# Kernel tuning notes

Measured on AMD Instinct MI355X. Metric: run time of the kernel, lower is better.

## Reference

```python
import jax, jax.numpy as jnp
import numpy as np

ALPHA = 10.0
DELTA = 0.0005
N = 16777216  # array_length


def setup_inputs() -> dict:
    key = jax.random.key(0)
    k1, k2 = jax.random.split(key)
    # learned parameter: in the original module this is initialized to linspace(0,1,N);
    # we use uniform [0,1] so the piecewise-linear search path is non-degenerate.
    indices = jax.random.uniform(k1, (N,), dtype=jnp.float32)
    array = jax.random.normal(k2, (N,), dtype=jnp.float32)
    return {"indices": indices, "array": array}


def reference(indices, array):
    # clamp learned knot positions to [0, 1]
    clamped = jnp.clip(indices, 0.0, 1.0)
    # piecewise-linear function f with x-knots = clamped, y-values = array.
    # jnp.interp requires ascending knots, so sort (x, y) pairs by x.
    order = jnp.argsort(clamped)
    xs = clamped[order]
    ys = array[order]
    # vectorized version of the per-index loop:
    #   left_item = f(clamped[i-1] + delta), this_item = f(clamped[i] - delta)
    q_left = clamped[:-1] + DELTA   # [N-1]
    q_this = clamped[1:] - DELTA    # [N-1]
    f_left = jnp.interp(q_left, xs, ys)
    f_this = jnp.interp(q_this, xs, ys)
    gap = jnp.maximum(f_left - f_this, 0.0)
    return ALPHA * jnp.sum(gap)
```

## Files before the change

### kernel.cpp

```cpp
#include <hip/hip_runtime.h>
#include <stdint.h>

#define ALPHA_C 10.0f
#define DELTA_C 0.0005f

typedef unsigned long long u64;
typedef unsigned u32;
typedef unsigned short u16;

#define KB2   (1u << 21)
#define NREG  8192
#define FPR   256
#define CAP   4096
#define DQ    137438953ULL
#define Q38MAX ((1ULL << 38) - 1)

#define OLDKB (1u << 22)
#define SCAN_BLOCKS 1024
#define SCAN_TPB 256
#define SCAN_PER_THREAD 16

__device__ __forceinline__ float clamp01(float x) {
    return fminf(fmaxf(x, 0.0f), 1.0f);
}
__device__ __forceinline__ u64 q38_of(float x) {
    double d = (double)clamp01(x) * 274877906944.0;
    u64 q = (u64)d;
    return q > Q38MAX ? Q38MAX : q;
}
__device__ __forceinline__ u16 f2bf(float f) {
    u32 b = __float_as_uint(f);
    return (u16)((b + 0x8000u) >> 16);
}
__device__ __forceinline__ float bf2f(u32 h) {
    return __uint_as_float(h << 16);
}


__global__ void __launch_bounds__(256) k_hist(const float* __restrict__ ind,
                                              u32* __restrict__ cnt8k, int n) {
    __shared__ u32 lh[NREG];
    for (int k = threadIdx.x; k < (int)NREG; k += 256) lh[k] = 0;
    __syncthreads();
    int stride = gridDim.x * blockDim.x;
    for (int i = blockIdx.x * blockDim.x + threadIdx.x; i < n; i += stride)
        atomicAdd(&lh[(u32)(q38_of(ind[i]) >> 25)], 1u);
    __syncthreads();
    for (int k = threadIdx.x; k < (int)NREG; k += 256) {
        u32 v = lh[k];
        if (v) atomicAdd(&cnt8k[k], v);
    }
}

__global__ void __launch_bounds__(1024) k_scan8k(u32* __restrict__ cnt8k) {
    __shared__ u32 lds[1024];
    int tid = threadIdx.x;
    int base = tid * 8;
    u32 v[8]; u32 tot = 0;
#pragma unroll
    for (int k = 0; k < 8; ++k) { v[k] = cnt8k[base + k]; tot += v[k]; }
    lds[tid] = tot;
    __syncthreads();
    u32 x = tot;
    for (int s = 1; s < 1024; s <<= 1) {
        u32 y = (tid >= s) ? lds[tid - s] : 0u;
        __syncthreads();
        x += y; lds[tid] = x;
        __syncthreads();
    }
    u32 run = x - tot;
#pragma unroll
    for (int k = 0; k < 8; ++k) { u32 c = v[k]; cnt8k[base + k] = run; run += c; }
}

__global__ void k_coarse(const float* __restrict__ ind, const float* __restrict__ arr,
                         u32* __restrict__ cnt8k,
                         u32* __restrict__ recx, u64* __restrict__ reciy, int n) {
    int i = blockIdx.x * blockDim.x + threadIdx.x;
    if (i < n) {
        float x = ind[i];
        u32 r = (u32)(q38_of(x) >> 25);
        u32 e = atomicAdd(&cnt8k[r], 1u);
        recx[e] = __float_as_uint(x);
        reciy[e] = ((u64)(u32)i << 16) | (u64)f2bf(arr[i]);
    }
}

__global__ void __launch_bounds__(256) k_fine(const u32* __restrict__ cnt8k,
                                              u32* __restrict__ foff,
                                              const u32* __restrict__ recx,
                                              u64* __restrict__ reciy_fdata) {
    __shared__ u32 sx[CAP];
    __shared__ u64 siy[CAP];
    __shared__ u32 incl[FPR];
    __shared__ u32 lexcl[FPR];
    __shared__ u32 lcnt[FPR];
    int r = blockIdx.x;
    u32 s = (r == 0) ? 0u : cnt8k[r - 1];
    u32 e = cnt8k[r];
    u32 cnt = e - s; if (cnt > CAP) cnt = CAP;
    for (u32 j = threadIdx.x; j < cnt; j += 256) { sx[j] = recx[s + j]; siy[j] = reciy_fdata[s + j]; }
    incl[threadIdx.x] = 0;
    lcnt[threadIdx.x] = 0;
    __syncthreads();
    for (u32 j = threadIdx.x; j < cnt; j += 256) {
        u32 lb = (u32)((q38_of(__uint_as_float(sx[j])) >> 17) & 255u);
        atomicAdd(&incl[lb], 1u);
    }
    __syncthreads();
    u32 myc = incl[threadIdx.x];
    u32 x = myc;
    for (int st = 1; st < 256; st <<= 1) {
        u32 y = (threadIdx.x >= (u32)st) ? incl[threadIdx.x - st] : 0u;
        __syncthreads();
        x += y; incl[threadIdx.x] = x;
        __syncthreads();
    }
    lexcl[threadIdx.x] = x - myc;
    foff[r * FPR + threadIdx.x] = s + x;
    __syncthreads();
    for (u32 j = threadIdx.x; j < cnt; j += 256) {
        u64 q = q38_of(__uint_as_float(sx[j]));
        u32 lb = (u32)((q >> 17) & 255u);
        u32 p = s + lexcl[lb] + atomicAdd(&lcnt[lb], 1u);
        u64 iy = siy[j];
        reciy_fdata[p] = ((q & 0x1FFFFULL) << 40) | ((iy & 0xFFFFULL) << 24) | (iy >> 16);
    }
}

__device__ float feval_q(u64 q, const u32* __restrict__ foff, const u64* __restrict__ fdata) {
    u32 qb = (u32)(q >> 17);
    u32 ql = (u32)(q & 0x1FFFFu);
    u32 s = qb ? foff[qb - 1] : 0u;
    u32 e = foff[qb];
    long long loQ = -1;
    u64 hiQ = ~0ULL;
    float loY = 0.0f, hiY = 0.0f;
    for (u32 p = s; p < e; ++p) {
        u64 d = fdata[p];
        u32 xlo = (u32)(d >> 40);
        u64 eq = ((u64)qb << 17) | xlo;
        float y = bf2f((u32)(d >> 24) & 0xFFFFu);
        if (xlo <= ql) { if ((long long)eq >= loQ) { loQ = (long long)eq; loY = y; } }
        else           { if (eq < hiQ)             { hiQ = eq;            hiY = y; } }
    }
    if (loQ < 0) {
        u32 bl = qb;
        while (bl > 0) {
            --bl;
            u32 s2 = bl ? foff[bl - 1] : 0u;
            u32 e2 = foff[bl];
            if (e2 > s2) {
                for (u32 p = s2; p < e2; ++p) {
                    u64 d = fdata[p];
                    u64 eq = ((u64)bl << 17) | (d >> 40);
                    if ((long long)eq >= loQ) { loQ = (long long)eq; loY = bf2f((u32)(d >> 24) & 0xFFFFu); }
                }
                break;
            }
        }
    }
    if (hiQ == ~0ULL) {
        u32 br = qb;
        while (br < KB2 - 1) {
            ++br;
            u32 s2 = foff[br - 1];
            u32 e2 = foff[br];
            if (e2 > s2) {
                for (u32 p = s2; p < e2; ++p) {
                    u64 d = fdata[p];
                    u64 eq = ((u64)br << 17) | (d >> 40);
                    if (eq < hiQ) { hiQ = eq; hiY = bf2f((u32)(d >> 24) & 0xFFFFu); }
                }
                break;
            }
        }
    }
    if (loQ < 0) return hiY;
    if (hiQ == ~0ULL) return loY;
    float dq = (float)(q - (u64)loQ);
    float dd = (float)(hiQ - (u64)loQ);
    return loY + (dq / dd) * (hiY - loY);
}

__global__ void __launch_bounds__(256) k_eval_t1(const u32* __restrict__ cnt8k,
        const u32* __restrict__ foff, const u64* __restrict__ fdata,
        u32* __restrict__ obcnt, u64* __restrict__ orec, float* __restrict__ fmEdge) {
    __shared__ u32 fend[FPR];
    int r = blockIdx.x;
    u32 s = r ? cnt8k[r - 1] : 0u;
    u32 e = cnt8k[r];
    fend[threadIdx.x] = foff[r * FPR + threadIdx.x];
    __syncthreads();
    for (u32 t = s + threadIdx.x; t < e; t += 256) {
        u64 d = fdata[t];
        u32 lo = 0;
#pragma unroll
        for (u32 st = 128; st; st >>= 1) if (t >= fend[lo + st - 1]) lo += st;
        u64 xq = (((u64)((u32)r * FPR + lo)) << 17) | (d >> 40);
        u32 i = (u32)(d & 0xFFFFFFu);
        u64 qp = xq + DQ; if (qp > Q38MAX) qp = Q38MAX;
        u64 qm = (xq >= DQ) ? xq - DQ : 0ULL;
        float fp = feval_q(qp, foff, fdata);
        float fm = feval_q(qm, foff, fdata);
        u32 bin = i >> 11;
        u32 sl = atomicAdd(&obcnt[bin], 1u);
        orec[((u64)bin << 11) + sl] = ((u64)i << 32) | ((u64)f2bf(fp) << 16) | (u64)f2bf(fm);
        if ((i & 2047u) == 0u) fmEdge[bin] = fm;
    }
}

__global__ void __launch_bounds__(256) k_eval_t2(const u32* __restrict__ cnt8k,
        const u32* __restrict__ foff, const u64* __restrict__ fdata,
        u32* __restrict__ oval) {
    __shared__ u32 fend[FPR];
    int r = blockIdx.x;
    u32 s = r ? cnt8k[r - 1] : 0u;
    u32 e = cnt8k[r];
    fend[threadIdx.x] = foff[r * FPR + threadIdx.x];
    __syncthreads();
    for (u32 t = s + threadIdx.x; t < e; t += 256) {
        u64 d = fdata[t];
        u32 lo = 0;
#pragma unroll
        for (u32 st = 128; st; st >>= 1) if (t >= fend[lo + st - 1]) lo += st;
        u64 xq = (((u64)((u32)r * FPR + lo)) << 17) | (d >> 40);
        u32 i = (u32)(d & 0xFFFFFFu);
        u64 qp = xq + DQ; if (qp > Q38MAX) qp = Q38MAX;
        u64 qm = (xq >= DQ) ? xq - DQ : 0ULL;
        float fp = feval_q(qp, foff, fdata);
        float fm = feval_q(qm, foff, fdata);
        oval[i] = ((u32)f2bf(fp) << 16) | (u32)f2bf(fm);
    }
}

__global__ void __launch_bounds__(256) k_pair1(const u64* __restrict__ orec,
        const float* __restrict__ fmEdge, float* __restrict__ out, int n) {
    __shared__ u32 v[2048];
    int r = blockIdx.x;
    long long base = (long long)r << 11;
    int cap = (int)((long long)n - base); if (cap > 2048) cap = 2048;
    for (int k = threadIdx.x; k < cap; k += 256) {
        u64 d = orec[base + k];
        v[(u32)(d >> 32) & 2047u] = (u32)d;
    }
    __syncthreads();
    float sum = 0.0f;
    for (int k = threadIdx.x; k < cap; k += 256) {
        long long gi = base + k;
        if (gi <= (long long)n - 2) {
            float fp = bf2f(v[k] >> 16);
            float fm = (k < 2047) ? bf2f(v[k + 1] & 0xFFFFu) : fmEdge[r + 1];
            sum += fmaxf(fp - fm, 0.0f);
        }
    }
    float w = sum;
    for (int s = 32; s > 0; s >>= 1) w += __shfl_down(w, s, 64);
    __shared__ float wsum[4];
    if ((threadIdx.x & 63) == 0) wsum[threadIdx.x >> 6] = w;
    __syncthreads();
    if (threadIdx.x == 0)
        atomicAdd(out, ALPHA_C * (wsum[0] + wsum[1] + wsum[2] + wsum[3]));
}

__global__ void __launch_bounds__(256) k_pair2(const u32* __restrict__ oval,
                                               float* __restrict__ out, int n) {
    int stride = gridDim.x * blockDim.x;
    float sum = 0.0f;
    for (int j = blockIdx.x * blockDim.x + threadIdx.x; j < n - 1; j += stride) {
        u32 a = oval[j], b = oval[j + 1];
        sum += fmaxf(bf2f(a >> 16) - bf2f(b & 0xFFFFu), 0.0f);
    }
    float w = sum;
    for (int s = 32; s > 0; s >>= 1) w += __shfl_down(w, s, 64);
    __shared__ float wsum[4];
    if ((threadIdx.x & 63) == 0) wsum[threadIdx.x >> 6] = w;
    __syncthreads();
    if (threadIdx.x == 0)
        atomicAdd(out, ALPHA_C * (wsum[0] + wsum[1] + wsum[2] + wsum[3]));
}


__device__ __forceinline__ int bucket_of(float x) {
    int b = (int)(x * (float)OLDKB);
    b = b < 0 ? 0 : b;
    b = b > (int)OLDKB - 1 ? (int)OLDKB - 1 : b;
    return b;
}

__global__ void scan1(u32* __restrict__ off, u32* __restrict__ bsums) {
    __shared__ u32 lds[SCAN_TPB];
    int base = blockIdx.x * (SCAN_TPB * SCAN_PER_THREAD) + threadIdx.x * SCAN_PER_THREAD;
    u32 v[SCAN_PER_THREAD];
    u32 tot = 0;
#pragma unroll
    for (int k = 0; k < SCAN_PER_THREAD; ++k) { v[k] = off[base + k]; tot += v[k]; }
    lds[threadIdx.x] = tot;
    __syncthreads();
    u32 x = tot;
    for (int s = 1; s < SCAN_TPB; s <<= 1) {
        u32 y = (threadIdx.x >= (u32)s) ? lds[threadIdx.x - s] : 0u;
        __syncthreads();
        x += y; lds[threadIdx.x] = x;
        __syncthreads();
    }
    if (threadIdx.x == SCAN_TPB - 1) bsums[blockIdx.x] = x;
    u32 run = x - tot;
#pragma unroll
    for (int k = 0; k < SCAN_PER_THREAD; ++k) { u32 c = v[k]; off[base + k] = run; run += c; }
}

__global__ void scan2(u32* __restrict__ bsums) {
    __shared__ u32 lds[SCAN_BLOCKS];
    int tid = threadIdx.x;
    u32 v = bsums[tid];
    lds[tid] = v;
    __syncthreads();
    u32 x = v;
    for (int s = 1; s < SCAN_BLOCKS; s <<= 1) {
        u32 y = (tid >= s) ? lds[tid - s] : 0u;
        __syncthreads();
        x += y; lds[tid] = x;
        __syncthreads();
    }
    bsums[tid] = x - v;
}

__global__ void scan3(u32* __restrict__ off, const u32* __restrict__ bsums) {
    int base = blockIdx.x * (SCAN_TPB * SCAN_PER_THREAD);
    u32 add = bsums[blockIdx.x];
#pragma unroll
    for (int k = 0; k < SCAN_PER_THREAD; ++k)
        off[base + k * SCAN_TPB + threadIdx.x] += add;
}

__global__ void hist_kernel(const float* __restrict__ ind, u32* __restrict__ off, int n) {
    int i = blockIdx.x * blockDim.x + threadIdx.x;
    if (i < n) atomicAdd(&off[bucket_of(clamp01(ind[i]))], 1u);
}

__global__ void scatter_kernel(const float* __restrict__ ind, const float* __restrict__ arr,
                               u32* __restrict__ off, float2* __restrict__ buck, int n) {
    int i = blockIdx.x * blockDim.x + threadIdx.x;
    if (i < n) {
        float x = clamp01(ind[i]);
        u32 p = atomicAdd(&off[bucket_of(x)], 1u);
        buck[p] = make_float2(x, arr[i]);
    }
}

__device__ float feval(float q, const u32* __restrict__ off, const float2* __restrict__ buck) {
    int b = bucket_of(q);
    u32 s = (b == 0) ? 0u : off[b - 1];
    u32 e = off[b];
    float loX = -1e30f, loY = 0.0f, hiX = 1e30f, hiY = 0.0f;
    for (u32 u = s; u < e; ++u) {
        float2 p = buck[u];
        if (p.x <= q) { if (p.x >= loX) { loX = p.x; loY = p.y; } }
        else          { if (p.x <  hiX) { hiX = p.x; hiY = p.y; } }
    }
    if (loX == -1e30f) {
        int bl = b;
        while (bl > 0) {
            --bl;
            u32 s2 = (bl == 0) ? 0u : off[bl - 1];
            u32 e2 = off[bl];
            if (e2 > s2) {
                for (u32 u = s2; u < e2; ++u) {
                    float2 p = buck[u];
                    if (p.x >= loX) { loX = p.x; loY = p.y; }
                }
                break;
            }
        }
    }
    if (hiX == 1e30f) {
        int br = b;
        while (br < (int)OLDKB - 1) {
            ++br;
            u32 s2 = off[br - 1];
            u32 e2 = off[br];
            if (e2 > s2) {
                for (u32 u = s2; u < e2; ++u) {
                    float2 p = buck[u];
                    if (p.x < hiX) { hiX = p.x; hiY = p.y; }
                }
                break;
            }
        }
    }
    if (loX == -1e30f) return hiY;
    if (hiX ==  1e30f) return loY;
    return loY + (q - loX) * (hiY - loY) / (hiX - loX);
}

__global__ void query_kernel(const float* __restrict__ ind, const u32* __restrict__ off,
                             const float2* __restrict__ buck, float* __restrict__ out, int nterm) {
    int j = blockIdx.x * blockDim.x + threadIdx.x;
    float term = 0.0f;
    if (j < nterm) {
        float c0 = clamp01(ind[j]);
        float c1 = clamp01(ind[j + 1]);
        float fa = feval(c0 + DELTA_C, off, buck);
        float fb = feval(c1 - DELTA_C, off, buck);
        term = fmaxf(fa - fb, 0.0f);
    }
    float w = term;
    for (int s = 32; s > 0; s >>= 1) w += __shfl_down(w, s, 64);
    __shared__ float wsum[4];
    if ((threadIdx.x & 63) == 0) wsum[threadIdx.x >> 6] = w;
    __syncthreads();
    if (threadIdx.x == 0) atomicAdd(out, ALPHA_C * (wsum[0] + wsum[1] + wsum[2] + wsum[3]));
}


extern "C" void kernel_launch(void* const* d_in, const int* in_sizes, int n_in,
                              void* d_out, int out_size, void* d_ws, size_t ws_size,
                              hipStream_t stream) {
    const float* ind = (const float*)d_in[0];
    const float* arr = (const float*)d_in[1];
    float* out = (float*)d_out;
    int n = in_sizes[0];

    const int tpb = 256;
    int nblk = (n + tpb - 1) / tpb;
    uint8_t* w = (uint8_t*)d_ws;

    const size_t FOFF_SZ = (size_t)KB2 * 4;
    const size_t AUX = (size_t)1 << 20;
    size_t SZ8 = (size_t)n * 8, SZ4 = (size_t)n * 4;
    size_t base = FOFF_SZ + AUX;
    size_t need_t2 = base + SZ8 + SZ4;
    size_t need_t1 = base + SZ8 + SZ8;

    if (n <= (1 << 24) && ws_size >= need_t2) {
        u32* foff   = (u32*)w;
        u32* cnt8k  = (u32*)(w + FOFF_SZ);
        u32* obcnt  = (u32*)(w + FOFF_SZ + 65536);
        float* fmEdge = (float*)(w + FOFF_SZ + 131072);
        u64* reciy  = (u64*)(w + base);
        u32* recx   = (u32*)(w + base + SZ8);
        u64* orec   = (u64*)recx;
        u32* oval   = (u32*)recx;

        bool t1 = (ws_size >= need_t1);

        hipMemsetAsync(cnt8k, 0, NREG * 4, stream);
        if (t1) hipMemsetAsync(obcnt, 0, NREG * 4, stream);
        hipMemsetAsync(out, 0, sizeof(float) * (size_t)out_size, stream);

        k_hist<<<512, 256, 0, stream>>>(ind, cnt8k, n);
        k_scan8k<<<1, 1024, 0, stream>>>(cnt8k);
        k_coarse<<<nblk, tpb, 0, stream>>>(ind, arr, cnt8k, recx, reciy, n);
        k_fine<<<NREG, 256, 0, stream>>>(cnt8k, foff, recx, reciy);
        if (t1) {
            k_eval_t1<<<NREG, 256, 0, stream>>>(cnt8k, foff, reciy, obcnt, orec, fmEdge);
            int nbins = (n + 2047) / 2048;
            k_pair1<<<nbins, 256, 0, stream>>>(orec, fmEdge, out, n);
        } else {
            k_eval_t2<<<NREG, 256, 0, stream>>>(cnt8k, foff, reciy, oval);
            k_pair2<<<2048, 256, 0, stream>>>(oval, out, n);
        }
    } else {
        const size_t FO = (size_t)OLDKB * 4;
        u32* off = (u32*)w;
        u32* bsums = (u32*)(w + FO);
        float2* buck = (float2*)(w + FO + 4096);

        hipMemsetAsync(off, 0, FO, stream);
        hipMemsetAsync(out, 0, sizeof(float) * (size_t)out_size, stream);

        hist_kernel<<<nblk, tpb, 0, stream>>>(ind, off, n);
        scan1<<<SCAN_BLOCKS, SCAN_TPB, 0, stream>>>(off, bsums);
        scan2<<<1, SCAN_BLOCKS, 0, stream>>>(bsums);
        scan3<<<SCAN_BLOCKS, SCAN_TPB, 0, stream>>>(off, bsums);
        scatter_kernel<<<nblk, tpb, 0, stream>>>(ind, arr, off, buck, n);
        int nterm = n - 1;
        query_kernel<<<(nterm + tpb - 1) / tpb, tpb, 0, stream>>>(ind, off, buck, out, nterm);
    }
}
```

Measured before the change: 1.742 ms.

## Double fine buckets, store 16-bit bucket offsets, drop scattered-output eval path

Doubles the number of fine buckets per region to 512, so each interpolation lookup scans fewer records, and stores the per-bucket offsets as 16-bit values relative to the region base. It also drops the t1 path (atomic binning plus the pair1 kernel) in favour of always writing oval directly and running pair2. Query points are now computed in float (x ± delta) instead of with a fixed-point delta, and ties are broken by index in the key to better match the reference. The costs are an extra cnt8k lookup per bucket range, 512-thread blocks in k_fine and k_eval, and a random scatter on the oval write.

```diff
diff --git a/kernel.cpp b/kernel.cpp
--- a/kernel.cpp
+++ b/kernel.cpp
@@ -8,11 +8,10 @@
 typedef unsigned u32;
 typedef unsigned short u16;
 
-#define KB2   (1u << 21)
+#define KB2   (1u << 22)
 #define NREG  8192
-#define FPR   256
+#define FPR   512
 #define CAP   4096
-#define DQ    137438953ULL
 #define Q38MAX ((1ULL << 38) - 1)
 
 #define OLDKB (1u << 22)
@@ -86,8 +85,8 @@
     }
 }
 
-__global__ void __launch_bounds__(256) k_fine(const u32* __restrict__ cnt8k,
-                                              u32* __restrict__ foff,
+__global__ void __launch_bounds__(512) k_fine(const u32* __restrict__ cnt8k,
+                                              u16* __restrict__ foff16,
                                               const u32* __restrict__ recx,
                                               u64* __restrict__ reciy_fdata) {
     __shared__ u32 sx[CAP];
@@ -99,168 +98,129 @@
     u32 s = (r == 0) ? 0u : cnt8k[r - 1];
     u32 e = cnt8k[r];
     u32 cnt = e - s; if (cnt > CAP) cnt = CAP;
-    for (u32 j = threadIdx.x; j < cnt; j += 256) { sx[j] = recx[s + j]; siy[j] = reciy_fdata[s + j]; }
+    for (u32 j = threadIdx.x; j < cnt; j += 512) { sx[j] = recx[s + j]; siy[j] = reciy_fdata[s + j]; }
     incl[threadIdx.x] = 0;
     lcnt[threadIdx.x] = 0;
     __syncthreads();
-    for (u32 j = threadIdx.x; j < cnt; j += 256) {
-        u32 lb = (u32)((q38_of(__uint_as_float(sx[j])) >> 17) & 255u);
+    for (u32 j = threadIdx.x; j < cnt; j += 512) {
+        u32 lb = (u32)((q38_of(__uint_as_float(sx[j])) >> 16) & (FPR - 1));
         atomicAdd(&incl[lb], 1u);
     }
     __syncthreads();
     u32 myc = incl[threadIdx.x];
     u32 x = myc;
-    for (int st = 1; st < 256; st <<= 1) {
+    for (int st = 1; st < FPR; st <<= 1) {
         u32 y = (threadIdx.x >= (u32)st) ? incl[threadIdx.x - st] : 0u;
         __syncthreads();
         x += y; incl[threadIdx.x] = x;
         __syncthreads();
     }
     lexcl[threadIdx.x] = x - myc;
-    foff[r * FPR + threadIdx.x] = s + x;
-    __syncthreads();
-    for (u32 j = threadIdx.x; j < cnt; j += 256) {
+    foff16[r * FPR + threadIdx.x] = (u16)x;
+    __syncthreads();
+    for (u32 j = threadIdx.x; j < cnt; j += 512) {
         u64 q = q38_of(__uint_as_float(sx[j]));
-        u32 lb = (u32)((q >> 17) & 255u);
+        u32 lb = (u32)((q >> 16) & (FPR - 1));
         u32 p = s + lexcl[lb] + atomicAdd(&lcnt[lb], 1u);
         u64 iy = siy[j];
-        reciy_fdata[p] = ((q & 0x1FFFFULL) << 40) | ((iy & 0xFFFFULL) << 24) | (iy >> 16);
-    }
-}
-
-__device__ float feval_q(u64 q, const u32* __restrict__ foff, const u64* __restrict__ fdata) {
-    u32 qb = (u32)(q >> 17);
-    u32 ql = (u32)(q & 0x1FFFFu);
-    u32 s = qb ? foff[qb - 1] : 0u;
-    u32 e = foff[qb];
-    long long loQ = -1;
-    u64 hiQ = ~0ULL;
+        reciy_fdata[p] = ((q & 0xFFFFULL) << 40) | ((iy & 0xFFFFULL) << 24) | (iy >> 16);
+    }
+}
+
+__device__ __forceinline__ void bucket_range(u32 b, const u32* __restrict__ cnt8k,
+                                             const u16* __restrict__ foff16,
+                                             u32* s, u32* e) {
+    u32 r = b >> 9;
+    u32 rbase = r ? cnt8k[r - 1] : 0u;
+    u32 lb = b & (FPR - 1);
+    *s = rbase + (lb ? (u32)foff16[b - 1] : 0u);
+    *e = rbase + (u32)foff16[b];
+}
+
+__device__ float feval_q(u64 qq, const u32* __restrict__ cnt8k,
+                         const u16* __restrict__ foff16, const u64* __restrict__ fdata) {
+    u32 qb = (u32)(qq >> 16);
+    u32 ql = (u32)(qq & 0xFFFFu);
+    u32 s, e;
+    bucket_range(qb, cnt8k, foff16, &s, &e);
+    long long loK = -1;
+    u64 hiK = ~0ULL;
     float loY = 0.0f, hiY = 0.0f;
     for (u32 p = s; p < e; ++p) {
         u64 d = fdata[p];
         u32 xlo = (u32)(d >> 40);
-        u64 eq = ((u64)qb << 17) | xlo;
+        u64 key = ((((u64)qb << 16) | xlo) << 24) | (d & 0xFFFFFFULL);
         float y = bf2f((u32)(d >> 24) & 0xFFFFu);
-        if (xlo <= ql) { if ((long long)eq >= loQ) { loQ = (long long)eq; loY = y; } }
-        else           { if (eq < hiQ)             { hiQ = eq;            hiY = y; } }
-    }
-    if (loQ < 0) {
+        if (xlo <= ql) { if ((long long)key >= loK) { loK = (long long)key; loY = y; } }
+        else           { if (key < hiK)             { hiK = key;            hiY = y; } }
+    }
+    if (loK < 0) {
         u32 bl = qb;
         while (bl > 0) {
             --bl;
-            u32 s2 = bl ? foff[bl - 1] : 0u;
-            u32 e2 = foff[bl];
+            u32 s2, e2;
+            bucket_range(bl, cnt8k, foff16, &s2, &e2);
             if (e2 > s2) {
                 for (u32 p = s2; p < e2; ++p) {
                     u64 d = fdata[p];
-                    u64 eq = ((u64)bl << 17) | (d >> 40);
-                    if ((long long)eq >= loQ) { loQ = (long long)eq; loY = bf2f((u32)(d >> 24) & 0xFFFFu); }
+                    u64 key = ((((u64)bl << 16) | (d >> 40)) << 24) | (d & 0xFFFFFFULL);
+                    if ((long long)key >= loK) { loK = (long long)key; loY = bf2f((u32)(d >> 24) & 0xFFFFu); }
                 }
                 break;
             }
         }
     }
-    if (hiQ == ~0ULL) {
+    if (hiK == ~0ULL) {
         u32 br = qb;
         while (br < KB2 - 1) {
             ++br;
-            u32 s2 = foff[br - 1];
-            u32 e2 = foff[br];
+            u32 s2, e2;
+            bucket_range(br, cnt8k, foff16, &s2, &e2);
             if (e2 > s2) {
                 for (u32 p = s2; p < e2; ++p) {
                     u64 d = fdata[p];
-                    u64 eq = ((u64)br << 17) | (d >> 40);
-                    if (eq < hiQ) { hiQ = eq; hiY = bf2f((u32)(d >> 24) & 0xFFFFu); }
+                    u64 key = ((((u64)br << 16) | (d >> 40)) << 24) | (d & 0xFFFFFFULL);
+                    if (key < hiK) { hiK = key; hiY = bf2f((u32)(d >> 24) & 0xFFFFu); }
                 }
                 break;
             }
         }
     }
-    if (loQ < 0) return hiY;
-    if (hiQ == ~0ULL) return loY;
-    float dq = (float)(q - (u64)loQ);
-    float dd = (float)(hiQ - (u64)loQ);
+    if (loK < 0) return hiY;
+    if (hiK == ~0ULL) return loY;
+    u64 loQ = (u64)loK >> 24;
+    u64 hiQ = hiK >> 24;
+    if (hiQ == loQ) return loY;
+    float dq = (float)(qq - loQ);
+    float dd = (float)(hiQ - loQ);
     return loY + (dq / dd) * (hiY - loY);
 }
 
-__global__ void __launch_bounds__(256) k_eval_t1(const u32* __restrict__ cnt8k,
-        const u32* __restrict__ foff, const u64* __restrict__ fdata,
-        u32* __restrict__ obcnt, u64* __restrict__ orec, float* __restrict__ fmEdge) {
-    __shared__ u32 fend[FPR];
-    int r = blockIdx.x;
-    u32 s = r ? cnt8k[r - 1] : 0u;
-    u32 e = cnt8k[r];
-    fend[threadIdx.x] = foff[r * FPR + threadIdx.x];
-    __syncthreads();
-    for (u32 t = s + threadIdx.x; t < e; t += 256) {
-        u64 d = fdata[t];
-        u32 lo = 0;
-#pragma unroll
-        for (u32 st = 128; st; st >>= 1) if (t >= fend[lo + st - 1]) lo += st;
-        u64 xq = (((u64)((u32)r * FPR + lo)) << 17) | (d >> 40);
-        u32 i = (u32)(d & 0xFFFFFFu);
-        u64 qp = xq + DQ; if (qp > Q38MAX) qp = Q38MAX;
-        u64 qm = (xq >= DQ) ? xq - DQ : 0ULL;
-        float fp = feval_q(qp, foff, fdata);
-        float fm = feval_q(qm, foff, fdata);
-        u32 bin = i >> 11;
-        u32 sl = atomicAdd(&obcnt[bin], 1u);
-        orec[((u64)bin << 11) + sl] = ((u64)i << 32) | ((u64)f2bf(fp) << 16) | (u64)f2bf(fm);
-        if ((i & 2047u) == 0u) fmEdge[bin] = fm;
-    }
-}
-
-__global__ void __launch_bounds__(256) k_eval_t2(const u32* __restrict__ cnt8k,
-        const u32* __restrict__ foff, const u64* __restrict__ fdata,
+__global__ void __launch_bounds__(512) k_eval(const u32* __restrict__ cnt8k,
+        const u16* __restrict__ foff16, const u64* __restrict__ fdata,
         u32* __restrict__ oval) {
     __shared__ u32 fend[FPR];
     int r = blockIdx.x;
     u32 s = r ? cnt8k[r - 1] : 0u;
     u32 e = cnt8k[r];
-    fend[threadIdx.x] = foff[r * FPR + threadIdx.x];
-    __syncthreads();
-    for (u32 t = s + threadIdx.x; t < e; t += 256) {
+    fend[threadIdx.x] = s + (u32)foff16[r * FPR + threadIdx.x];
+    __syncthreads();
+    for (u32 t = s + threadIdx.x; t < e; t += 512) {
         u64 d = fdata[t];
         u32 lo = 0;
 #pragma unroll
-        for (u32 st = 128; st; st >>= 1) if (t >= fend[lo + st - 1]) lo += st;
-        u64 xq = (((u64)((u32)r * FPR + lo)) << 17) | (d >> 40);
+        for (u32 st = 256; st; st >>= 1) if (t >= fend[lo + st - 1]) lo += st;
+        u64 xq = (((u64)((u32)r * FPR + lo)) << 16) | (d >> 40);
         u32 i = (u32)(d & 0xFFFFFFu);
-        u64 qp = xq + DQ; if (qp > Q38MAX) qp = Q38MAX;
-        u64 qm = (xq >= DQ) ? xq - DQ : 0ULL;
-        float fp = feval_q(qp, foff, fdata);
-        float fm = feval_q(qm, foff, fdata);
+        float x = (float)((double)xq * 3.63797880709171295e-12);
+        float qpf = x + DELTA_C;
+        float qmf = x - DELTA_C;
+        u64 qp = q38_of(qpf);
+        u64 qm = q38_of(qmf);
+        float fp = feval_q(qp, cnt8k, foff16, fdata);
+        float fm = feval_q(qm, cnt8k, foff16, fdata);
         oval[i] = ((u32)f2bf(fp) << 16) | (u32)f2bf(fm);
     }
-}
-
-__global__ void __launch_bounds__(256) k_pair1(const u64* __restrict__ orec,
-        const float* __restrict__ fmEdge, float* __restrict__ out, int n) {
-    __shared__ u32 v[2048];
-    int r = blockIdx.x;
-    long long base = (long long)r << 11;
-    int cap = (int)((long long)n - base); if (cap > 2048) cap = 2048;
-    for (int k = threadIdx.x; k < cap; k += 256) {
-        u64 d = orec[base + k];
-        v[(u32)(d >> 32) & 2047u] = (u32)d;
-    }
-    __syncthreads();
-    float sum = 0.0f;
-    for (int k = threadIdx.x; k < cap; k += 256) {
-        long long gi = base + k;
-        if (gi <= (long long)n - 2) {
-            float fp = bf2f(v[k] >> 16);
-            float fm = (k < 2047) ? bf2f(v[k + 1] & 0xFFFFu) : fmEdge[r + 1];
-            sum += fmaxf(fp - fm, 0.0f);
-        }
-    }
-    float w = sum;
-    for (int s = 32; s > 0; s >>= 1) w += __shfl_down(w, s, 64);
-    __shared__ float wsum[4];
-    if ((threadIdx.x & 63) == 0) wsum[threadIdx.x >> 6] = w;
-    __syncthreads();
-    if (threadIdx.x == 0)
-        atomicAdd(out, ALPHA_C * (wsum[0] + wsum[1] + wsum[2] + wsum[3]));
 }
 
 __global__ void __launch_bounds__(256) k_pair2(const u32* __restrict__ oval,
@@ -426,41 +386,28 @@
     int nblk = (n + tpb - 1) / tpb;
     uint8_t* w = (uint8_t*)d_ws;
 
-    const size_t FOFF_SZ = (size_t)KB2 * 4;
+    const size_t FOFF_SZ = (size_t)KB2 * 2;
     const size_t AUX = (size_t)1 << 20;
     size_t SZ8 = (size_t)n * 8, SZ4 = (size_t)n * 4;
     size_t base = FOFF_SZ + AUX;
-    size_t need_t2 = base + SZ8 + SZ4;
-    size_t need_t1 = base + SZ8 + SZ8;
-
-    if (n <= (1 << 24) && ws_size >= need_t2) {
-        u32* foff   = (u32*)w;
+    size_t need = base + SZ8 + SZ4;
+
+    if (n <= (1 << 24) && ws_size >= need) {
+        u16* foff16 = (u16*)w;
         u32* cnt8k  = (u32*)(w + FOFF_SZ);
-        u32* obcnt  = (u32*)(w + FOFF_SZ + 65536);
-        float* fmEdge = (float*)(w + FOFF_SZ + 131072);
         u64* reciy  = (u64*)(w + base);
         u32* recx   = (u32*)(w + base + SZ8);
-        u64* orec   = (u64*)recx;
         u32* oval   = (u32*)recx;
 
-        bool t1 = (ws_size >= need_t1);
-
         hipMemsetAsync(cnt8k, 0, NREG * 4, stream);
-        if (t1) hipMemsetAsync(obcnt, 0, NREG * 4, stream);
         hipMemsetAsync(out, 0, sizeof(float) * (size_t)out_size, stream);
 
         k_hist<<<512, 256, 0, stream>>>(ind, cnt8k, n);
         k_scan8k<<<1, 1024, 0, stream>>>(cnt8k);
         k_coarse<<<nblk, tpb, 0, stream>>>(ind, arr, cnt8k, recx, reciy, n);
-        k_fine<<<NREG, 256, 0, stream>>>(cnt8k, foff, recx, reciy);
-        if (t1) {
-            k_eval_t1<<<NREG, 256, 0, stream>>>(cnt8k, foff, reciy, obcnt, orec, fmEdge);
-            int nbins = (n + 2047) / 2048;
-            k_pair1<<<nbins, 256, 0, stream>>>(orec, fmEdge, out, n);
-        } else {
-            k_eval_t2<<<NREG, 256, 0, stream>>>(cnt8k, foff, reciy, oval);
-            k_pair2<<<2048, 256, 0, stream>>>(oval, out, n);
-        }
+        k_fine<<<NREG, 512, 0, stream>>>(cnt8k, foff16, recx, reciy);
+        k_eval<<<NREG, 512, 0, stream>>>(cnt8k, foff16, reciy, oval);
+        k_pair2<<<2048, 256, 0, stream>>>(oval, out, n);
     } else {
         const size_t FO = (size_t)OLDKB * 4;
         u32* off = (u32*)w;
```

Measured after the change: 1.611 ms. -7.5%, faster.
